# Optimization experiments

Hardware: AMD Instinct MI355X
Metric: run time of the kernel (lower is better)

Reference implementation:

```python
import jax, jax.numpy as jnp
import numpy as np

DIM = 384
HEADS = 12
WS = (2, 7, 7)
SS = (1, 3, 3)
B, D, H, W = 4, 8, 56, 56
N = WS[0] * WS[1] * WS[2]  # 98


def _win_part_np(x, ws):
    b, d, h, w, c = x.shape
    x = x.reshape(b, d // ws[0], ws[0], h // ws[1], ws[1], w // ws[2], ws[2], c)
    return x.transpose(0, 1, 3, 5, 2, 4, 6, 7).reshape(-1, ws[0] * ws[1] * ws[2], c)


def setup_inputs() -> dict:
    key = jax.random.key(0)
    ks = jax.random.split(key, 6)
    s = 0.02
    x = jax.random.normal(ks[0], (B, D, H, W, DIM), jnp.float32)
    # relative position index (static int buffer)
    coords = np.stack(np.meshgrid(np.arange(WS[0]), np.arange(WS[1]), np.arange(WS[2]), indexing='ij')).reshape(3, -1)
    rel = (coords[:, :, None] - coords[:, None, :]).transpose(1, 2, 0)
    rel[..., 0] += WS[0] - 1
    rel[..., 1] += WS[1] - 1
    rel[..., 2] += WS[2] - 1
    rel[..., 0] *= (2 * WS[1] - 1) * (2 * WS[2] - 1)
    rel[..., 1] *= 2 * WS[2] - 1
    rel_index = jnp.asarray(rel.sum(-1), jnp.int32)  # [N, N]
    # shifted-window attention mask (standard Swin construction)
    img = np.zeros((1, D, H, W, 1), np.float32)
    cnt = 0
    for dsl in (slice(0, -WS[0]), slice(-WS[0], -SS[0]), slice(-SS[0], None)):
        for hsl in (slice(0, -WS[1]), slice(-WS[1], -SS[1]), slice(-SS[1], None)):
            for wsl in (slice(0, -WS[2]), slice(-WS[2], -SS[2]), slice(-SS[2], None)):
                img[:, dsl, hsl, wsl, :] = cnt
                cnt += 1
    mw = _win_part_np(img, WS).squeeze(-1)  # [nW, N]
    attn_mask = np.where(mw[:, None, :] != mw[:, :, None], -100.0, 0.0).astype(np.float32)
    table_size = (2 * WS[0] - 1) * (2 * WS[1] - 1) * (2 * WS[2] - 1)
    return {
        'x': x,
        'mask': jnp.asarray(attn_mask),
        'rel_table': jax.random.normal(ks[1], (table_size, HEADS), jnp.float32) * s,
        'rel_index': rel_index,
        'qkv_w': jax.random.normal(ks[2], (3 * DIM, DIM), jnp.float32) * s,
        'qkv_b': jnp.zeros((3 * DIM,), jnp.float32),
        'proj_w': jax.random.normal(ks[3], (DIM, DIM), jnp.float32) * s,
        'proj_b': jnp.zeros((DIM,), jnp.float32),
        'g1': jnp.ones((DIM,), jnp.float32), 'b1': jnp.zeros((DIM,), jnp.float32),
        'g2': jnp.ones((DIM,), jnp.float32), 'b2': jnp.zeros((DIM,), jnp.float32),
        'fc1_w': jax.random.normal(ks[4], (DIM, DIM), jnp.float32) * s,
        'fc1_b': jnp.zeros((DIM,), jnp.float32),
        'fc2_w': jax.random.normal(ks[5], (DIM, DIM), jnp.float32) * s,
        'fc2_b': jnp.zeros((DIM,), jnp.float32),
    }


def _ln(x, g, b, eps=1e-5):
    mu = x.mean(-1, keepdims=True)
    var = jnp.mean((x - mu) ** 2, axis=-1, keepdims=True)
    return (x - mu) * jax.lax.rsqrt(var + eps) * g + b


def _window_partition(x, ws):
    b, d, h, w, c = x.shape
    x = x.reshape(b, d // ws[0], ws[0], h // ws[1], ws[1], w // ws[2], ws[2], c)
    return x.transpose(0, 1, 3, 5, 2, 4, 6, 7).reshape(-1, ws[0] * ws[1] * ws[2], c)


def _window_reverse(win, ws, b, d, h, w):
    x = win.reshape(b, d // ws[0], h // ws[1], w // ws[2], ws[0], ws[1], ws[2], -1)
    return x.transpose(0, 1, 4, 2, 5, 3, 6, 7).reshape(b, d, h, w, -1)


def reference(x, mask, rel_table, rel_index, qkv_w, qkv_b, proj_w, proj_b,
              g1, b1, g2, b2, fc1_w, fc1_b, fc2_w, fc2_b):
    shortcut = x
    h = _ln(x, g1, b1)
    b, d, hh, ww, c = h.shape
    # get_window_size: clamp window/shift to input extents (static here)
    ws = [min(WS[i], (d, hh, ww)[i]) for i in range(3)]
    ss = [0 if (d, hh, ww)[i] <= WS[i] else SS[i] for i in range(3)]
    pad = [(ws[i] - (d, hh, ww)[i] % ws[i]) % ws[i] for i in range(3)]
    h = jnp.pad(h, ((0, 0), (0, pad[0]), (0, pad[1]), (0, pad[2]), (0, 0)))
    dp, hp, wp = h.shape[1:4]
    if any(ss):
        h = jnp.roll(h, shift=(-ss[0], -ss[1], -ss[2]), axis=(1, 2, 3))
    xw = _window_partition(h, ws)  # [B_, N, C]
    bw, n, _ = xw.shape
    hd = c // HEADS
    qkv = (xw @ qkv_w.T + qkv_b).reshape(bw, n, 3, HEADS, hd).transpose(2, 0, 3, 1, 4)
    q, k, v = qkv[0], qkv[1], qkv[2]  # [B_, H, N, hd]
    scale = hd ** -0.5
    attn = jnp.einsum('bhnd,bhmd->bhnm', q * scale, k)
    bias = rel_table[rel_index[:n, :n].reshape(-1)].reshape(n, n, HEADS).transpose(2, 0, 1)
    attn = attn + bias[None]
    nW = mask.shape[0]
    attn = attn.reshape(bw // nW, nW, HEADS, n, n) + mask[None, :, None]
    attn = jax.nn.softmax(attn.reshape(bw, HEADS, n, n), axis=-1)
    out = jnp.einsum('bhnm,bhmd->bhnd', attn, v).transpose(0, 2, 1, 3).reshape(bw, n, c)
    out = out @ proj_w.T + proj_b
    out = _window_reverse(out, ws, b, dp, hp, wp)
    if any(ss):
        out = jnp.roll(out, shift=(ss[0], ss[1], ss[2]), axis=(1, 2, 3))
    out = out[:, :d, :hh, :ww, :]
    x1 = shortcut + out
    h2 = _ln(x1, g2, b2)
    mlp = jax.nn.gelu(h2 @ fc1_w.T + fc1_b, approximate=False) @ fc2_w.T + fc2_b
    return x1 + mlp
```

## Files before the change

kernel.cpp:

```cpp
#include <hip/hip_runtime.h>
#include <hip/hip_bf16.h>

#define HEADS 12
#define NWIN 1024
#define NW_MASK 256
#define NTOK 98
#define CDIM 384
#define NROWS (NWIN * NTOK)
#define QKVN (3 * CDIM)
#define PSTR 136
#define LOG2E 1.4426950408889634f
#define SCALE_LOG2E 0.25503486f

using u16 = unsigned short;
typedef __attribute__((ext_vector_type(8))) short short8;
typedef __attribute__((ext_vector_type(4))) short s16x4;
typedef __attribute__((ext_vector_type(4))) float f32x4;
typedef __attribute__((ext_vector_type(2))) unsigned u32x2;

__device__ __forceinline__ float b2f(u16 u) { return __uint_as_float(((unsigned)u) << 16); }
__device__ __forceinline__ u16 f2b(float f) {
  unsigned u = __float_as_uint(f);
  u += 0x7FFF + ((u >> 16) & 1);
  return (u16)(u >> 16);
}

__device__ __forceinline__ int tok_of_row(int r) {
  int win = r / NTOK;
  int j   = r - win * NTOK;
  int b   = win >> 8;
  int wl  = win & 255;
  int wd = wl >> 6, wh = (wl >> 3) & 7, ww = wl & 7;
  int od = j / 49; int rem = j - od * 49;
  int oh = rem / 7; int ow = rem - oh * 7;
  int sd = (wd * 2 + od + 1) & 7;
  int sh = wh * 7 + oh + 3; if (sh >= 56) sh -= 56;
  int sw = ww * 7 + ow + 3; if (sw >= 56) sw -= 56;
  return ((b * 8 + sd) * 56 + sh) * 56 + sw;
}

__device__ __forceinline__ int xcd_swz(int bid, int nwg) {
  int q = nwg >> 3, r = nwg & 7;
  int xcd = bid & 7, i = bid >> 3;
  return ((xcd < r) ? xcd * (q + 1) : r * (q + 1) + (xcd - r) * q) + i;
}

__global__ void detect_kernel(const unsigned* __restrict__ g1w, int* __restrict__ flag) {
  if (threadIdx.x == 0 && blockIdx.x == 0)
    flag[0] = (g1w[0] == 0x3F800000u) ? 1 : 0;
}

__device__ __forceinline__ float raw_at(const void* src, size_t j, int isf32) {
  return isf32 ? ((const float*)src)[j] : b2f(((const u16*)src)[j]);
}

struct CvtArgs {
  const void* src[12];
  unsigned off[13];
};
__global__ __launch_bounds__(256) void cvt_all(CvtArgs a, u16* __restrict__ dst,
                                               const int* __restrict__ flag) {
  int i = blockIdx.x * 256 + threadIdx.x;
  if (i >= (int)a.off[12]) return;
  int s = 0;
#pragma unroll
  for (int k = 1; k < 12; ++k) s += (i >= (int)a.off[k]);
  int j = i - (int)a.off[s];
  dst[i] = flag[0] ? f2b(((const float*)a.src[s])[j]) : ((const u16*)a.src[s])[j];
}

__global__ __launch_bounds__(256) void ln_kernel(const void* __restrict__ in,
                                                 const u16* __restrict__ gam,
                                                 const u16* __restrict__ bet,
                                                 u16* __restrict__ outp,
                                                 const int* __restrict__ flag) {
  int wrow = blockIdx.x * 4 + (threadIdx.x >> 6);
  int lane = threadIdx.x & 63;
  int isf32 = flag[0];
  size_t srow = (size_t)tok_of_row(wrow);
  const u16*   ip16 = (const u16*)in + srow * CDIM;
  const float* ip32 = (const float*)in + srow * CDIM;
  float xv[6]; float s = 0.f, s2 = 0.f;
#pragma unroll
  for (int i = 0; i < 6; ++i) {
    int c = lane + 64 * i;
    xv[i] = isf32 ? ip32[c] : b2f(ip16[c]);
    s += xv[i]; s2 += xv[i] * xv[i];
  }
#pragma unroll
  for (int off = 1; off < 64; off <<= 1) {
    s  += __shfl_xor(s, off);
    s2 += __shfl_xor(s2, off);
  }
  float mu = s * (1.f / CDIM);
  float var = s2 * (1.f / CDIM) - mu * mu;
  float rstd = rsqrtf(var + 1e-5f);
  u16* op = outp + (size_t)wrow * CDIM;
#pragma unroll
  for (int i = 0; i < 6; ++i) {
    int c = lane + 64 * i;
    op[c] = f2b((xv[i] - mu) * rstd * b2f(gam[c]) + b2f(bet[c]));
  }
}

__global__ void bias_kernel(const void* __restrict__ tab, const int* __restrict__ idx,
                            float* __restrict__ biasf, const int* __restrict__ flag) {
  int i = blockIdx.x * 256 + threadIdx.x;
  if (i >= HEADS * NTOK * 100) return;
  int isf32 = flag[0];
  int h = i / (NTOK * 100);
  int rem = i - h * (NTOK * 100);
  int q = rem / 100, t = rem - q * 100;
  biasf[i] = (t < NTOK) ? raw_at(tab, (size_t)idx[q * NTOK + t] * HEADS + h, isf32) * LOG2E : 0.f;
}

__global__ void maskp_kernel(const void* __restrict__ msrc, u16* __restrict__ mdst,
                             const int* __restrict__ flag, float* __restrict__ st2) {
  int i = blockIdx.x * 256 + threadIdx.x;
  if (i < 2 * NROWS) st2[i] = 0.f;
  if (i >= NW_MASK * NTOK * 100) return;
  int isf32 = flag[0];
  int w = i / (NTOK * 100);
  int rem = i - w * (NTOK * 100);
  int q = rem / 100, t = rem - q * 100;
  mdst[i] = (t < NTOK) ? f2b(raw_at(msrc, (size_t)(w * NTOK + q) * NTOK + t, isf32) * LOG2E)
                       : (u16)0;
}

__device__ __forceinline__ void gload16(const u16* g, u16* l) {
  __builtin_amdgcn_global_load_lds((const __attribute__((address_space(1))) unsigned*)g,
                                   (__attribute__((address_space(3))) unsigned*)l,
                                   16, 0, 0);
}

template<int EPI, bool SWZ>
__global__ __launch_bounds__(256) void gemm_bt(const u16* __restrict__ A, int lda,
                                               const u16* __restrict__ W,
                                               const u16* __restrict__ bias,
                                               int NB, void* __restrict__ outb, int ldo,
                                               const void* __restrict__ aux,
                                               const int* __restrict__ flag,
                                               float* __restrict__ stats,
                                               const u16* __restrict__ lng,
                                               const u16* __restrict__ lnb) {
  __shared__ __align__(16) u16 lA[128 * 32];
  __shared__ __align__(16) u16 lB[128 * 32];
  int bid = SWZ ? xcd_swz(blockIdx.x, gridDim.x) : blockIdx.x;
  int mb = bid / NB, nb = bid - mb * NB;
  int row0 = mb * 128, col0 = nb * 128;
  int tid = threadIdx.x;
  int lane = tid & 63;
  int wid = tid >> 6;
  int wr = (wid >> 1) * 64, wc = (wid & 1) * 64;
  f32x4 zero = {0.f, 0.f, 0.f, 0.f};
  f32x4 acc[4][4];
#pragma unroll
  for (int m = 0; m < 4; ++m)
#pragma unroll
    for (int n = 0; n < 4; ++n) acc[m][n] = zero;

  int e0 = tid * 8;
  int e1 = 2048 + tid * 8;
  int r0 = e0 >> 5, c0 = e0 & 31;
  int r1 = e1 >> 5, c1 = e1 & 31;
  int g = (lane >> 4) * 8, fr = lane & 15;

  float mu_[4], rs_[4];
  if (EPI == 2) {
#pragma unroll
    for (int m = 0; m < 4; ++m) {
      int rr = row0 + wr + m * 16 + fr;
      float sv = stats[2 * rr], qv = stats[2 * rr + 1];
      float mu = sv * (1.f / CDIM);
      float var = qv * (1.f / CDIM) - mu * mu;
      mu_[m] = mu;
      rs_[m] = rsqrtf(var + 1e-5f);
    }
  }

  for (int kt = 0; kt < CDIM; kt += 32) {
    gload16(&A[(size_t)(row0 + r0) * lda + kt + c0], &lA[e0]);
    gload16(&A[(size_t)(row0 + r1) * lda + kt + c1], &lA[e1]);
    gload16(&W[(size_t)(col0 + r0) * CDIM + kt + c0], &lB[e0]);
    gload16(&W[(size_t)(col0 + r1) * CDIM + kt + c1], &lB[e1]);
    __syncthreads();
    short8 af[4], bf[4];
#pragma unroll
    for (int m = 0; m < 4; ++m) af[m] = *(const short8*)&lA[(wr + m * 16 + fr) * 32 + g];
#pragma unroll
    for (int n = 0; n < 4; ++n) bf[n] = *(const short8*)&lB[(wc + n * 16 + fr) * 32 + g];
    if (EPI == 2) {
      short8 gv = *(const short8*)&lng[kt + g];
      short8 bv8 = *(const short8*)&lnb[kt + g];
#pragma unroll
      for (int m = 0; m < 4; ++m) {
        short8 a = af[m], o;
#pragma unroll
        for (int i = 0; i < 8; ++i) {
          float f = (b2f((u16)a[i]) - mu_[m]) * rs_[m] * b2f((u16)gv[i]) + b2f((u16)bv8[i]);
          o[i] = (short)f2b(f);
        }
        af[m] = o;
      }
    }
#pragma unroll
    for (int m = 0; m < 4; ++m)
#pragma unroll
      for (int n = 0; n < 4; ++n)
        acc[m][n] = __builtin_amdgcn_mfma_f32_16x16x32_bf16(af[m], bf[n], acc[m][n], 0, 0, 0);
    __syncthreads();
  }

  int isf32 = (EPI == 1 || EPI == 3) ? flag[0] : 0;
  int colo = lane & 15;
  int rowo = (lane >> 4) * 4;
  float bv[4];
#pragma unroll
  for (int n = 0; n < 4; ++n) bv[n] = b2f(bias[col0 + wc + n * 16 + colo]);
#pragma unroll
  for (int m = 0; m < 4; ++m) {
#pragma unroll
    for (int r = 0; r < 4; ++r) {
      int gr = row0 + wr + m * 16 + rowo + r;
      int t = (EPI == 1 || EPI == 3) ? tok_of_row(gr) : 0;
      float ps = 0.f, ps2 = 0.f;
#pragma unroll
      for (int n = 0; n < 4; ++n) {
        int gc = col0 + wc + n * 16 + colo;
        float v = acc[m][n][r] + bv[n];
        if (EPI == 0) {
          ((u16*)outb)[(size_t)gr * ldo + gc] = f2b(v);
        } else if (EPI == 1) {
          float xs = isf32 ? ((const float*)aux)[(size_t)t * CDIM + gc]
                           : b2f(((const u16*)aux)[(size_t)t * CDIM + gc]);
          float o = v + xs;
          ((u16*)outb)[(size_t)gr * ldo + gc] = f2b(o);
          ps += o; ps2 += o * o;
        } else if (EPI == 2) {
          float ge = 0.5f * v * (1.f + erff(v * 0.70710678118654752f));
          ((u16*)outb)[(size_t)gr * ldo + gc] = f2b(ge);
        } else {
          float x1v = b2f(((const u16*)aux)[(size_t)gr * CDIM + gc]);
          float o = v + x1v;
          if (isf32) ((float*)outb)[(size_t)t * CDIM + gc] = o;
          else       ((u16*)outb)[(size_t)t * CDIM + gc] = f2b(o);
        }
      }
      if (EPI == 1) {
#pragma unroll
        for (int off = 1; off < 16; off <<= 1) {
          ps  += __shfl_xor(ps, off);
          ps2 += __shfl_xor(ps2, off);
        }
        if (colo == 0) {
          atomicAdd(&stats[2 * gr],     ps);
          atomicAdd(&stats[2 * gr + 1], ps2);
        }
      }
    }
  }
}

__global__ __launch_bounds__(256, 3) void attn_mfma(u16* __restrict__ qkv,
                                                    const u16* __restrict__ maskp,
                                                    const float* __restrict__ biasf) {
  __shared__ __align__(16) u16 P4[4][16 * PSTR];
  int wid = threadIdx.x >> 6, lane = threadIdx.x & 63;
  int gh = blockIdx.x * 4 + wid;
  int win = gh / HEADS, hd = gh - win * HEADS;
  int l15 = lane & 15, g = lane >> 4;
  u16* P = P4[wid];
  const size_t base = (size_t)win * NTOK * QKVN + (size_t)hd * 32;
  u16* qp = qkv + base;
  const u16* kp = qkv + base + CDIM;
  const u16* vp = qkv + base + 2 * CDIM;
  const f32x4 zero = {0.f, 0.f, 0.f, 0.f};

  { u32x2 z = {0u, 0u}; *(u32x2*)&P[l15 * PSTR + 112 + 4 * g] = z; }

  short8 kf[7];
#pragma unroll
  for (int n = 0; n < 7; ++n) {
    int tok = n * 16 + l15; if (tok > NTOK - 1) tok = NTOK - 1;
    kf[n] = *(const short8*)&kp[(size_t)tok * QKVN + 8 * g];
  }
  short8 vf[2][4];
#pragma unroll
  for (int kk = 0; kk < 4; ++kk)
#pragma unroll
    for (int i = 0; i < 8; ++i) {
      int tok = 32 * kk + 8 * g + i;
      const u16* vr = vp + (size_t)tok * QKVN + l15;
      u16 v0 = (tok < NTOK) ? vr[0]  : (u16)0;
      u16 v1 = (tok < NTOK) ? vr[16] : (u16)0;
      vf[0][kk][i] = (short)v0;
      vf[1][kk][i] = (short)v1;
    }

  const float* brow = biasf + (size_t)hd * NTOK * 100;
  const u16*   mrow = maskp + (size_t)(win & (NW_MASK - 1)) * NTOK * 100;

  for (int m = 0; m < 7; ++m) {
    int qrow = m * 16 + l15;
    int qr = qrow > NTOK - 1 ? NTOK - 1 : qrow;
    short8 qf = *(const short8*)&qp[(size_t)qr * QKVN + 8 * g];
    f32x4 st[7];
#pragma unroll
    for (int n = 0; n < 7; ++n)
      st[n] = __builtin_amdgcn_mfma_f32_16x16x32_bf16(kf[n], qf, zero, 0, 0, 0);

    float pv[7][4];
    float mx = -1e30f;
#pragma unroll
    for (int n = 0; n < 7; ++n) {
      f32x4 bb = *(const f32x4*)&brow[(size_t)qr * 100 + n * 16 + 4 * g];
      s16x4 mm = *(const s16x4*)&mrow[(size_t)qr * 100 + n * 16 + 4 * g];
#pragma unroll
      for (int r = 0; r < 4; ++r) {
        int tok = n * 16 + 4 * g + r;
        float s = st[n][r] * SCALE_LOG2E + bb[r] + b2f((u16)mm[r]);
        if (tok > NTOK - 1) s = -1e30f;
        pv[n][r] = s;
        mx = fmaxf(mx, s);
      }
    }
    mx = fmaxf(mx, __shfl_xor(mx, 16));
    mx = fmaxf(mx, __shfl_xor(mx, 32));
    float sum = 0.f;
#pragma unroll
    for (int n = 0; n < 7; ++n)
#pragma unroll
      for (int r = 0; r < 4; ++r) {
        float e = exp2f(pv[n][r] - mx);
        pv[n][r] = e; sum += e;
      }
    sum += __shfl_xor(sum, 16);
    sum += __shfl_xor(sum, 32);
    float inv = 1.f / sum;
#pragma unroll
    for (int n = 0; n < 7; ++n) {
      __hip_bfloat162 h0 = __float22bfloat162_rn(make_float2(pv[n][0] * inv, pv[n][1] * inv));
      __hip_bfloat162 h1 = __float22bfloat162_rn(make_float2(pv[n][2] * inv, pv[n][3] * inv));
      u32x2 wv = { *(unsigned*)&h0, *(unsigned*)&h1 };
      *(u32x2*)&P[l15 * PSTR + n * 16 + 4 * g] = wv;
    }
    f32x4 oa0 = zero, oa1 = zero;
#pragma unroll
    for (int kk = 0; kk < 4; ++kk) {
      short8 pf = *(const short8*)&P[l15 * PSTR + kk * 32 + 8 * g];
      oa0 = __builtin_amdgcn_mfma_f32_16x16x32_bf16(pf, vf[0][kk], oa0, 0, 0, 0);
      oa1 = __builtin_amdgcn_mfma_f32_16x16x32_bf16(pf, vf[1][kk], oa1, 0, 0, 0);
    }
#pragma unroll
    for (int r = 0; r < 4; ++r) {
      int row = m * 16 + 4 * g + r;
      if (row < NTOK) {
        qp[(size_t)row * QKVN + l15]      = f2b(oa0[r]);
        qp[(size_t)row * QKVN + 16 + l15] = f2b(oa1[r]);
      }
    }
  }
}

extern "C" void kernel_launch(void* const* d_in, const int* in_sizes, int n_in,
                              void* d_out, int out_size, void* d_ws, size_t ws_size,
                              hipStream_t stream) {
  (void)n_in; (void)out_size; (void)ws_size;
  const void* x    = d_in[0];
  const int* ridx  = (const int*)d_in[3];

  char* ws = (char*)d_ws;
  const size_t SZ_QKV = (size_t)NROWS * QKVN * 2;
  const size_t SZ_MAT = (size_t)NROWS * CDIM * 2;
  const size_t SZ_BIAS = (size_t)HEADS * NTOK * 100 * 4;
  const size_t SZ_MASKP = (size_t)NW_MASK * NTOK * 100 * 2;
  u16* qkv     = (u16*)ws;
  u16* bufA    = (u16*)(ws + SZ_QKV);
  u16* bufX1   = (u16*)(ws + SZ_QKV + SZ_MAT);
  float* biasf = (float*)(ws + SZ_QKV + 2 * SZ_MAT);
  u16* maskp   = (u16*)(ws + SZ_QKV + 2 * SZ_MAT + SZ_BIAS);
  int* flag    = (int*)(ws + SZ_QKV + 2 * SZ_MAT + SZ_BIAS + SZ_MASKP);
  u16* cvt     = (u16*)((char*)flag + 256);
  float* stats2 = (float*)((char*)flag + 256 + 2 * 1024 * 1024);

  detect_kernel<<<1, 64, 0, stream>>>((const unsigned*)d_in[8], flag);

  CvtArgs ca;
  unsigned off = 0;
  u16* cp[16];
  for (int k = 0; k < 12; ++k) {
    int i = 4 + k;
    ca.src[k] = d_in[i];
    ca.off[k] = off;
    cp[i] = cvt + off;
    off += (unsigned)in_sizes[i];
  }
  ca.off[12] = off;
  cvt_all<<<(off + 255) / 256, 256, 0, stream>>>(ca, cvt, flag);

  bias_kernel<<<(HEADS * NTOK * 100 + 255) / 256, 256, 0, stream>>>(d_in[2], ridx, biasf, flag);
  maskp_kernel<<<(NW_MASK * NTOK * 100 + 255) / 256, 256, 0, stream>>>(d_in[1], maskp, flag, stats2);
  ln_kernel<<<NROWS / 4, 256, 0, stream>>>(x, cp[8], cp[9], bufA, flag);
  gemm_bt<0, true><<<(NROWS / 128) * (QKVN / 128), 256, 0, stream>>>(
      bufA, CDIM, cp[4], cp[5], QKVN / 128, qkv, QKVN, nullptr, flag, nullptr, nullptr, nullptr);
  attn_mfma<<<(NWIN * HEADS) / 4, 256, 0, stream>>>(qkv, maskp, biasf);
  gemm_bt<1, false><<<(NROWS / 128) * (CDIM / 128), 256, 0, stream>>>(
      qkv, QKVN, cp[6], cp[7], CDIM / 128, bufX1, CDIM, x, flag, stats2, nullptr, nullptr);
  gemm_bt<2, false><<<(NROWS / 128) * (CDIM / 128), 256, 0, stream>>>(
      bufX1, CDIM, cp[12], cp[13], CDIM / 128, bufA, CDIM, nullptr, flag, stats2, cp[10], cp[11]);
  gemm_bt<3, false><<<(NROWS / 128) * (CDIM / 128), 256, 0, stream>>>(
      bufA, CDIM, cp[14], cp[15], CDIM / 128, d_out, CDIM, bufX1, flag, nullptr, nullptr, nullptr);
}
```

Before: 779.4 us.

## Triple-buffer GEMM LDS tiles with async prefetch and XOR-swizzled layout

Replaces the single-buffer load-sync-compute loop in the shared GEMM kernel with a three-stage LDS ring. Tiles are prefetched two k-steps ahead via global_load_lds, using explicit vmcnt waits and a single barrier per step. Global source columns are also XOR-swizzled so the fragment reads from LDS avoid bank conflicts. The cost is triple the LDS footprint (48KB per block), which may reduce occupancy, and the code now relies on hand-tuned waitcnt counts.

```diff
diff --git a/kernel.cpp b/kernel.cpp
--- a/kernel.cpp
+++ b/kernel.cpp
@@ -11,6 +11,7 @@
 #define PSTR 136
 #define LOG2E 1.4426950408889634f
 #define SCALE_LOG2E 0.25503486f
+#define KSTEPS 12
 
 using u16 = unsigned short;
 typedef __attribute__((ext_vector_type(8))) short short8;
@@ -143,8 +144,8 @@
                                                float* __restrict__ stats,
                                                const u16* __restrict__ lng,
                                                const u16* __restrict__ lnb) {
-  __shared__ __align__(16) u16 lA[128 * 32];
-  __shared__ __align__(16) u16 lB[128 * 32];
+  __shared__ __align__(16) u16 lA[3][128 * 32];
+  __shared__ __align__(16) u16 lB[3][128 * 32];
   int bid = SWZ ? xcd_swz(blockIdx.x, gridDim.x) : blockIdx.x;
   int mb = bid / NB, nb = bid - mb * NB;
   int row0 = mb * 128, col0 = nb * 128;
@@ -159,11 +160,17 @@
 #pragma unroll
     for (int n = 0; n < 4; ++n) acc[m][n] = zero;
 
-  int e0 = tid * 8;
-  int e1 = 2048 + tid * 8;
-  int r0 = e0 >> 5, c0 = e0 & 31;
-  int r1 = e1 >> 5, c1 = e1 & 31;
+  int r0 = tid >> 2, s0 = tid & 3;
+  int r1 = 64 + r0;
+  int c0 = 8 * (s0 ^ ((r0 >> 1) & 3));
+  int c1 = 8 * (s0 ^ ((r1 >> 1) & 3));
+  const u16* Ab0 = &A[(size_t)(row0 + r0) * lda + c0];
+  const u16* Ab1 = &A[(size_t)(row0 + r1) * lda + c1];
+  const u16* Wb0 = &W[(size_t)(col0 + r0) * CDIM + c0];
+  const u16* Wb1 = &W[(size_t)(col0 + r1) * CDIM + c1];
+  int e0 = tid * 8, e1 = 2048 + tid * 8;
   int g = (lane >> 4) * 8, fr = lane & 15;
+  int sw = 8 * ((lane >> 4) ^ ((fr >> 1) & 3));
 
   float mu_[4], rs_[4];
   if (EPI == 2) {
@@ -178,20 +185,34 @@
     }
   }
 
-  for (int kt = 0; kt < CDIM; kt += 32) {
-    gload16(&A[(size_t)(row0 + r0) * lda + kt + c0], &lA[e0]);
-    gload16(&A[(size_t)(row0 + r1) * lda + kt + c1], &lA[e1]);
-    gload16(&W[(size_t)(col0 + r0) * CDIM + kt + c0], &lB[e0]);
-    gload16(&W[(size_t)(col0 + r1) * CDIM + kt + c1], &lB[e1]);
-    __syncthreads();
+#define STAGE(t, b)                                  \
+  {                                                  \
+    int kt = (t) * 32;                               \
+    gload16(Ab0 + kt, &lA[b][e0]);                   \
+    gload16(Ab1 + kt, &lA[b][e1]);                   \
+    gload16(Wb0 + kt, &lB[b][e0]);                   \
+    gload16(Wb1 + kt, &lB[b][e1]);                   \
+  }
+
+  STAGE(0, 0);
+  STAGE(1, 1);
+
+#pragma unroll
+  for (int t = 0; t < KSTEPS; ++t) {
+    int cur = t % 3;
+    if (t < KSTEPS - 1) asm volatile("s_waitcnt vmcnt(4)" ::: "memory");
+    else                asm volatile("s_waitcnt vmcnt(0)" ::: "memory");
+    __builtin_amdgcn_s_barrier();
+    if (t + 2 < KSTEPS) STAGE(t + 2, (t + 2) % 3);
+
     short8 af[4], bf[4];
 #pragma unroll
-    for (int m = 0; m < 4; ++m) af[m] = *(const short8*)&lA[(wr + m * 16 + fr) * 32 + g];
-#pragma unroll
-    for (int n = 0; n < 4; ++n) bf[n] = *(const short8*)&lB[(wc + n * 16 + fr) * 32 + g];
+    for (int m = 0; m < 4; ++m) af[m] = *(const short8*)&lA[cur][(wr + m * 16 + fr) * 32 + sw];
+#pragma unroll
+    for (int n = 0; n < 4; ++n) bf[n] = *(const short8*)&lB[cur][(wc + n * 16 + fr) * 32 + sw];
     if (EPI == 2) {
-      short8 gv = *(const short8*)&lng[kt + g];
-      short8 bv8 = *(const short8*)&lnb[kt + g];
+      short8 gv = *(const short8*)&lng[t * 32 + g];
+      short8 bv8 = *(const short8*)&lnb[t * 32 + g];
 #pragma unroll
       for (int m = 0; m < 4; ++m) {
         short8 a = af[m], o;
@@ -208,8 +229,8 @@
 #pragma unroll
       for (int n = 0; n < 4; ++n)
         acc[m][n] = __builtin_amdgcn_mfma_f32_16x16x32_bf16(af[m], bf[n], acc[m][n], 0, 0, 0);
-    __syncthreads();
-  }
+  }
+#undef STAGE
 
   int isf32 = (EPI == 1 || EPI == 3) ? flag[0] : 0;
   int colo = lane & 15;
```

Result: slower. 853.9 us (+9.6%).
